# Kernel optimization log

Hardware: AMD Instinct MI355X
Metric: run time of the kernel (lower is better)

Reference implementation:

```python
import jax, jax.numpy as jnp
import numpy as np

B, T, E, QKV, H = 2, 2048, 1024, 1024, 16
DH = QKV // H
R_LAYER = 2

def rmsnorm(x):
    eps = jnp.finfo(x.dtype).eps
    return x * jax.lax.rsqrt(jnp.mean(x * x, axis=-1, keepdims=True) + eps)

def w_norm(w, n):
    # scale whole matrix so its (unbiased) std matches n**-0.5
    std = jnp.std(w, ddof=1)
    return w * (n ** -0.5 / (std + 1e-8))

def rotary(x, cos, sin):
    d = x.shape[-1] // 2
    x1, x2 = x[..., :d], x[..., d:]
    return jnp.concatenate([x1 * cos + x2 * sin, -x1 * sin + x2 * cos], axis=-1)

def w_split(w):
    w_qkv = w[:3 * QKV]                               # (3*QKV, E)
    w_sw = w[3 * QKV:5 * QKV].reshape(2 * E, QKV)     # (2*E, QKV)
    w_out = w[5 * QKV:]                               # (E, E)
    return w_qkv, w_sw, w_out

def aft(x, w_qkv):
    qkv = rmsnorm(x) @ w_qkv.T                        # (B,T,3*QKV)
    q, k, v = jnp.split(qkv, 3, axis=-1)
    q, k = rmsnorm(q), rmsnorm(k)
    wexp = jnp.exp(k)
    kv_c = jnp.cumsum(wexp * v, axis=1)
    w_c = jnp.cumsum(wexp, axis=1)
    y = jax.nn.sigmoid(q) * kv_c / (w_c + 1e-6)
    return x, y

def tea(x, cos, sin, w_qkv):
    qkv = (rmsnorm(x) @ w_qkv.T).reshape(B, T, H, 3 * DH)
    q, k, v = jnp.split(qkv, 3, axis=-1)              # each (B,T,H,DH)
    q, k = rotary(q, cos, sin), rotary(k, cos, sin)
    q, k = rmsnorm(q), rmsnorm(k)
    q = q.transpose(0, 2, 1, 3)                       # (B,H,T,DH)
    k = k.transpose(0, 2, 1, 3)
    v = v.transpose(0, 2, 1, 3)
    scores = jnp.einsum('bhqd,bhkd->bhqk', q, k) * DH ** -0.5
    mask = jnp.tril(jnp.ones((T, T), dtype=bool))
    scores = jnp.where(mask, scores, -jnp.inf)
    att = jax.nn.softmax(scores, axis=-1)
    y = jnp.einsum('bhqk,bhkd->bhqd', att, v)
    return x, y.transpose(0, 2, 1, 3).reshape(B, T, QKV)

def swiglu(x, y, w_sw, w_out, ret_oa=True):
    uv = y @ w_sw.T                                   # (B,T,2*E)
    u, v = jnp.split(uv, 2, axis=-1)
    out = x + (u * jax.nn.silu(v)) @ w_out.T
    if not ret_oa:
        return out
    o = rmsnorm(u.reshape(B * T, -1))
    a = v.reshape(B * T, -1)
    oa = jax.nn.softmax((o.T @ a) * E ** -0.5, axis=-1)  # (E,E)
    return out, oa

def setup_inputs():
    key = jax.random.key(0)
    k1, k2 = jax.random.split(key)
    x = jax.random.normal(k1, (B, T, E), dtype=jnp.float32)
    s = 3 ** 0.5 * E ** -0.5
    w = jax.random.uniform(k2, (5 * QKV + E, E), dtype=jnp.float32, minval=-s, maxval=s)
    half = DH // 2
    inv_freq = 1.0 / (10000.0 ** (jnp.arange(half, dtype=jnp.float32) / half))
    freqs = jnp.outer(jnp.arange(T, dtype=jnp.float32), inv_freq)  # (T, half)
    cos = jnp.cos(freqs)[:, None, :]                  # (T,1,half) broadcasts over (B,T,H,half)
    sin = jnp.sin(freqs)[:, None, :]
    return {"x": x, "w": w, "cos": cos, "sin": sin}

def reference(x, w, cos, sin):
    for i in range(R_LAYER):
        w_qkv, w_sw, w_out = w_split(w)
        w_qkv = w_norm(w_qkv, E)
        w_sw = w_norm(w_sw, QKV)
        w_out = w_norm(w_out, E)
        if (i + 1) % 4 == 0:
            x, y = tea(x, cos, sin, w_qkv)
        else:
            x, y = aft(x, w_qkv)
        x, oa = swiglu(x, y, w_sw, w_out, ret_oa=True)
        # RetentionMechanism.forward: hypernetwork weight mixing
        wT = w_norm(w @ oa, 5 * QKV + E)
        w = wT * jax.nn.silu(w) + w
    w_qkv, w_sw, w_out = w_split(w)                   # note: no w_norm on final split (matches source)
    x, y = tea(x, cos, sin, w_qkv)
    return swiglu(x, y, w_sw, w_out, ret_oa=False)
```

## Files before the change

### kernel.cpp

```cpp
#include <hip/hip_runtime.h>
#include <hip/hip_bf16.h>
#include <math.h>

#define TPB 256

constexpr int Bc = 2, Tc = 2048, Ec = 1024, QKVc = 1024, Hc = 16, DHc = 64;
constexpr long BT = (long)Bc * Tc;
constexpr int WR = 5 * QKVc + Ec;
constexpr float F32_EPS = 1.1920928955078125e-07f;
constexpr int NCH = 64, CHL = Tc / NCH;

typedef __attribute__((ext_vector_type(8))) short short8;
typedef __attribute__((ext_vector_type(4))) float f32x4;

__device__ __forceinline__ unsigned short f2bu(float f) {
    union { __hip_bfloat16 h; unsigned short u; } c; c.h = __float2bfloat16(f); return c.u;
}
__device__ __forceinline__ float bu2f(unsigned short u) {
    union { __hip_bfloat16 h; unsigned short u; } c; c.u = u; return __bfloat162float(c.h);
}
__device__ __forceinline__ float ldval(const float* p) { return *p; }
__device__ __forceinline__ float ldval(const unsigned short* p) { return bu2f(*p); }

__device__ __forceinline__ void gload_lds16(const void* g, void* l) {
    __builtin_amdgcn_global_load_lds((const __attribute__((address_space(1))) void*)g,
                                     (__attribute__((address_space(3))) void*)l, 16, 0, 0);
}

template<int CTRL>
__device__ __forceinline__ float dppf(float x) {
    union { float f; int i; } a, b;
    a.f = x;
    b.i = __builtin_amdgcn_update_dpp(0, a.i, CTRL, 0xF, 0xF, true);
    return b.f;
}
__device__ __forceinline__ float max16(float v) {
    v = fmaxf(v, dppf<0xB1>(v));
    v = fmaxf(v, dppf<0x4E>(v));
    v = fmaxf(v, dppf<0x124>(v));
    v = fmaxf(v, dppf<0x128>(v));
    return v;
}
__device__ __forceinline__ float sum16(float v) {
    v += dppf<0xB1>(v);
    v += dppf<0x4E>(v);
    v += dppf<0x124>(v);
    v += dppf<0x128>(v);
    return v;
}

__global__ void k_std_partial3(const float* __restrict__ w, float* __restrict__ out) {
    __shared__ float ls[TPB], lss[TPB];
    int seg = blockIdx.y;
    long base = (seg == 0) ? 0L : (seg == 1 ? 3072L * 1024 : 5120L * 1024);
    long n    = (seg == 0) ? 3072L * 1024 : (seg == 1 ? 2048L * 1024 : 1024L * 1024);
    const float* p = w + base;
    float s = 0.f, ss = 0.f;
    for (long i = (long)blockIdx.x * TPB + threadIdx.x; i < n; i += 256L * TPB) {
        float v = p[i]; s += v; ss += v * v;
    }
    ls[threadIdx.x] = s; lss[threadIdx.x] = ss; __syncthreads();
    for (int o = 128; o > 0; o >>= 1) {
        if (threadIdx.x < o) { ls[threadIdx.x] += ls[threadIdx.x + o]; lss[threadIdx.x] += lss[threadIdx.x + o]; }
        __syncthreads();
    }
    if (threadIdx.x == 0) { out[seg * 512 + blockIdx.x] = ls[0]; out[seg * 512 + 256 + blockIdx.x] = lss[0]; }
}

__global__ void k_std_final3(const float* __restrict__ part, float* __restrict__ scales) {
    __shared__ float ls[TPB], lss[TPB];
    for (int seg = 0; seg < 3; ++seg) {
        ls[threadIdx.x] = part[seg * 512 + threadIdx.x];
        lss[threadIdx.x] = part[seg * 512 + 256 + threadIdx.x];
        __syncthreads();
        for (int o = 128; o > 0; o >>= 1) {
            if (threadIdx.x < o) { ls[threadIdx.x] += ls[threadIdx.x + o]; lss[threadIdx.x] += lss[threadIdx.x + o]; }
            __syncthreads();
        }
        if (threadIdx.x == 0) {
            float n = (seg == 0) ? 3145728.0f : (seg == 1 ? 2097152.0f : 1048576.0f);
            float var = (lss[0] - ls[0] * ls[0] / n) / (n - 1.0f);
            scales[seg] = 0.03125f / (sqrtf(fmaxf(var, 0.0f)) + 1e-8f);
        }
        __syncthreads();
    }
}

__global__ void k_std_partial(const float* __restrict__ p, long n, float* __restrict__ out) {
    __shared__ float ls[TPB], lss[TPB];
    float s = 0.f, ss = 0.f;
    for (long i = (long)blockIdx.x * TPB + threadIdx.x; i < n; i += (long)gridDim.x * TPB) {
        float v = p[i]; s += v; ss += v * v;
    }
    ls[threadIdx.x] = s; lss[threadIdx.x] = ss; __syncthreads();
    for (int o = 128; o > 0; o >>= 1) {
        if (threadIdx.x < o) { ls[threadIdx.x] += ls[threadIdx.x + o]; lss[threadIdx.x] += lss[threadIdx.x + o]; }
        __syncthreads();
    }
    if (threadIdx.x == 0) { out[blockIdx.x] = ls[0]; out[gridDim.x + blockIdx.x] = lss[0]; }
}

__global__ void k_std_final(const float* __restrict__ part, float n, float rs, float* __restrict__ scale) {
    __shared__ float ls[TPB], lss[TPB];
    ls[threadIdx.x] = part[threadIdx.x];
    lss[threadIdx.x] = part[TPB + threadIdx.x];
    __syncthreads();
    for (int o = 128; o > 0; o >>= 1) {
        if (threadIdx.x < o) { ls[threadIdx.x] += ls[threadIdx.x + o]; lss[threadIdx.x] += lss[threadIdx.x + o]; }
        __syncthreads();
    }
    if (threadIdx.x == 0) {
        float var = (lss[0] - ls[0] * ls[0] / n) / (n - 1.0f);
        scale[0] = rs / (sqrtf(fmaxf(var, 0.0f)) + 1e-8f);
    }
}

__global__ void k_rms_qk(unsigned short* __restrict__ qkv) {
    __shared__ float red[TPB];
    int bid = blockIdx.x;
    long row = bid >> 1; int half = bid & 1;
    unsigned short* p = qkv + row * 3072 + half * 1024;
    ushort4 v = *(const ushort4*)(p + threadIdx.x * 4);
    float f0 = bu2f(v.x), f1 = bu2f(v.y), f2 = bu2f(v.z), f3 = bu2f(v.w);
    red[threadIdx.x] = f0 * f0 + f1 * f1 + f2 * f2 + f3 * f3;
    __syncthreads();
    for (int o = 128; o > 0; o >>= 1) {
        if (threadIdx.x < o) red[threadIdx.x] += red[threadIdx.x + o];
        __syncthreads();
    }
    float sc = rsqrtf(red[0] / 1024.0f + F32_EPS);
    ushort4 o4; o4.x = f2bu(f0 * sc); o4.y = f2bu(f1 * sc); o4.z = f2bu(f2 * sc); o4.w = f2bu(f3 * sc);
    *(ushort4*)(p + threadIdx.x * 4) = o4;
}

__global__ void k_rms1024b(const float* __restrict__ in, unsigned short* __restrict__ out, long ldin, long ldout) {
    __shared__ float red[TPB];
    long row = blockIdx.x;
    float4 v = *(const float4*)(in + row * ldin + threadIdx.x * 4);
    float ss = v.x * v.x + v.y * v.y + v.z * v.z + v.w * v.w;
    red[threadIdx.x] = ss; __syncthreads();
    for (int o = 128; o > 0; o >>= 1) {
        if (threadIdx.x < o) red[threadIdx.x] += red[threadIdx.x + o];
        __syncthreads();
    }
    float sc = rsqrtf(red[0] / 1024.0f + F32_EPS);
    ushort4 o4; o4.x = f2bu(v.x * sc); o4.y = f2bu(v.y * sc); o4.z = f2bu(v.z * sc); o4.w = f2bu(v.w * sc);
    *(ushort4*)(out + row * ldout + threadIdx.x * 4) = o4;
}

__global__ void k_cast_bf16(const float* __restrict__ in, unsigned short* __restrict__ out, long n4) {
    long i = (long)blockIdx.x * TPB + threadIdx.x;
    if (i >= n4) return;
    float4 v = *(const float4*)(in + i * 4);
    ushort4 o; o.x = f2bu(v.x); o.y = f2bu(v.y); o.z = f2bu(v.z); o.w = f2bu(v.w);
    *(ushort4*)(out + i * 4) = o;
}

template<typename TI>
__global__ void k_tcast(const TI* __restrict__ in, long ldi, long sIn,
                        unsigned short* __restrict__ out, long ldo, long sOut,
                        const float* __restrict__ rowscale) {
    __shared__ float tile[64][65];
    const TI* ip = in + (long)blockIdx.z * sIn;
    unsigned short* op = out + (long)blockIdx.z * sOut;
    int r0 = blockIdx.y * 64, c0 = blockIdx.x * 64;
    int tid = threadIdx.x;
    int rr = tid >> 4, cc = (tid & 15) * 4;
    #pragma unroll
    for (int u = 0; u < 4; ++u) {
        int r = rr + u * 16;
        float sc = rowscale ? rowscale[r0 + r] : 1.0f;
        #pragma unroll
        for (int j = 0; j < 4; ++j)
            tile[r][cc + j] = ldval(ip + (long)(r0 + r) * ldi + c0 + cc + j) * sc;
    }
    __syncthreads();
    #pragma unroll
    for (int u = 0; u < 4; ++u) {
        int c = rr + u * 16;
        ushort4 o;
        o.x = f2bu(tile[cc + 0][c]); o.y = f2bu(tile[cc + 1][c]);
        o.z = f2bu(tile[cc + 2][c]); o.w = f2bu(tile[cc + 3][c]);
        *(ushort4*)(op + (long)(c0 + c) * ldo + r0 + cc) = o;
    }
}

__global__ void k_tcast2(const unsigned short* __restrict__ uv, const float* __restrict__ uscale,
                         unsigned short* __restrict__ t1, unsigned short* __restrict__ t2) {
    __shared__ float tile[64][65];
    int z = blockIdx.z;
    const unsigned short* ip = uv + (z ? 1024 : 0);
    unsigned short* op = z ? t2 : t1;
    int r0 = blockIdx.y * 64, c0 = blockIdx.x * 64;
    int tid = threadIdx.x;
    int rr = tid >> 4, cc = (tid & 15) * 4;
    #pragma unroll
    for (int u = 0; u < 4; ++u) {
        int r = rr + u * 16;
        float sc = z ? 1.0f : uscale[r0 + r];
        ushort4 v = *(const ushort4*)(ip + (long)(r0 + r) * 2048 + c0 + cc);
        tile[r][cc + 0] = bu2f(v.x) * sc; tile[r][cc + 1] = bu2f(v.y) * sc;
        tile[r][cc + 2] = bu2f(v.z) * sc; tile[r][cc + 3] = bu2f(v.w) * sc;
    }
    __syncthreads();
    #pragma unroll
    for (int u = 0; u < 4; ++u) {
        int c = rr + u * 16;
        ushort4 o;
        o.x = f2bu(tile[cc + 0][c]); o.y = f2bu(tile[cc + 1][c]);
        o.z = f2bu(tile[cc + 2][c]); o.w = f2bu(tile[cc + 3][c]);
        *(ushort4*)(op + (long)(c0 + c) * 4096 + r0 + cc) = o;
    }
}

template<int WRITE_BF16>
__global__ __launch_bounds__(256)
void k_bgemm(int K,
             const unsigned short* __restrict__ A, int lda, long sA,
             const unsigned short* __restrict__ B, int ldb, long sB,
             void* __restrict__ C, int ldc, long sCi, long sSplit, int nsplit,
             const float* __restrict__ scale_ptr, float fscale,
             const float* __restrict__ addp, int ldadd) {
    __shared__ unsigned short Asl[128 * 64];
    __shared__ unsigned short Bsl[128 * 64];
    int bz = blockIdx.z;
    int batch = bz, sp = 0;
    if (nsplit > 1) { batch = bz / nsplit; sp = bz - batch * nsplit; }
    int m0 = blockIdx.y * 128, n0 = blockIdx.x * 128;
    const unsigned short* Ap = A + (long)batch * sA + (long)sp * K;
    const unsigned short* Bp = B + (long)batch * sB + (long)sp * K;
    int tid = threadIdx.x, lane = tid & 63, wave = tid >> 6;
    int wr = wave >> 1, wc = wave & 1;
    f32x4 acc[4][4] = {};
    for (int k0 = 0; k0 < K; k0 += 64) {
        #pragma unroll
        for (int cc = 0; cc < 4; ++cc) {
            int bu = (wave * 4 + cc) * 64;
            int uidx = bu + lane;
            int r = uidx >> 3, slot = uidx & 7;
            int gu = slot ^ (r & 7);
            gload_lds16(Ap + (long)(m0 + r) * lda + k0 + gu * 8, Asl + bu * 8);
        }
        #pragma unroll
        for (int cc = 0; cc < 4; ++cc) {
            int bu = (wave * 4 + cc) * 64;
            int uidx = bu + lane;
            int r = uidx >> 3, slot = uidx & 7;
            int gu = slot ^ (r & 7);
            gload_lds16(Bp + (long)(n0 + r) * ldb + k0 + gu * 8, Bsl + bu * 8);
        }
        __syncthreads();
        #pragma unroll
        for (int ksub = 0; ksub < 2; ++ksub) {
            short8 av[4], bv[4];
            #pragma unroll
            for (int m = 0; m < 4; ++m) {
                int r = wr * 64 + m * 16 + (lane & 15);
                int slot = (ksub * 4 + (lane >> 4)) ^ (r & 7);
                av[m] = *(const short8*)(Asl + r * 64 + slot * 8);
            }
            #pragma unroll
            for (int n = 0; n < 4; ++n) {
                int r = wc * 64 + n * 16 + (lane & 15);
                int slot = (ksub * 4 + (lane >> 4)) ^ (r & 7);
                bv[n] = *(const short8*)(Bsl + r * 64 + slot * 8);
            }
            #pragma unroll
            for (int m = 0; m < 4; ++m)
                #pragma unroll
                for (int n = 0; n < 4; ++n)
                    acc[m][n] = __builtin_amdgcn_mfma_f32_16x16x32_bf16(av[m], bv[n], acc[m][n], 0, 0, 0);
        }
        __syncthreads();
    }
    float s = fscale * (scale_ptr ? scale_ptr[0] : 1.0f);
    long cbase = (long)batch * sCi + (long)sp * sSplit;
    int row0 = m0 + wr * 64, col0 = n0 + wc * 64 + (lane & 15);
    int rbase = (lane >> 4) * 4;
    #pragma unroll
    for (int m = 0; m < 4; ++m)
        #pragma unroll
        for (int i = 0; i < 4; ++i) {
            long row = row0 + m * 16 + rbase + i;
            #pragma unroll
            for (int n = 0; n < 4; ++n) {
                long col = col0 + n * 16;
                float v = acc[m][n][i] * s;
                if (addp) v += addp[row * (long)ldadd + col];
                long idx = cbase + row * ldc + col;
                if (WRITE_BF16) ((unsigned short*)C)[idx] = f2bu(v);
                else ((float*)C)[idx] = v;
            }
        }
}

__global__ __launch_bounds__(256)
void k_flash_split(const unsigned short* __restrict__ hq, const unsigned short* __restrict__ hk,
                   const unsigned short* __restrict__ hvT,
                   unsigned short* __restrict__ opart, float* __restrict__ mpart, float* __restrict__ lpart) {
    __shared__ unsigned short P_lds[4][32 * 72];
    int lane = threadIdx.x & 63, wave = threadIdx.x >> 6;
    unsigned short* P = P_lds[wave];
    int g = lane >> 4, c = lane & 15;
    unsigned bid = blockIdx.x;
    unsigned bswz = (bid & 7) * 160 + (bid >> 3);
    unsigned gi = bswz * 4 + wave;
    unsigned bh = gi / 160, itr = gi % 160;
    int item = 159 - (int)itr;
    int strip, chunk;
    if (item < 16)      { strip = item;                 chunk = 0; }
    else if (item < 48) { strip = 16 + (item - 16) / 2; chunk = (item - 16) & 1; }
    else if (item < 96) { strip = 32 + (item - 48) / 3; chunk = (item - 48) % 3; }
    else                { strip = 48 + (item - 96) / 4; chunk = (item - 96) & 3; }
    int q0 = strip * 32;
    int nt = (q0 + 32 + 63) >> 6;
    int ti0 = chunk * 8;
    int ti1 = ti0 + 8 < nt ? ti0 + 8 : nt;
    const unsigned short* qb = hq + (long)bh * Tc * 64;
    const unsigned short* kb = hk + (long)bh * Tc * 64;
    const unsigned short* vtb = hvT + (long)bh * 64 * Tc;

    short8 qf[2][2];
    #pragma unroll
    for (int mf = 0; mf < 2; ++mf)
        #pragma unroll
        for (int ks = 0; ks < 2; ++ks)
            qf[mf][ks] = *(const short8*)(qb + (long)(q0 + mf * 16 + c) * 64 + ks * 32 + g * 8);

    f32x4 o_acc[2][4] = {};
    float m_run[2][4], lpp[2][4];
    #pragma unroll
    for (int mf = 0; mf < 2; ++mf)
        #pragma unroll
        for (int i = 0; i < 4; ++i) { m_run[mf][i] = -3.0e38f; lpp[mf][i] = 0.f; }

    short8 kcur[2][4];
    #pragma unroll
    for (int ks = 0; ks < 2; ++ks)
        #pragma unroll
        for (int nf = 0; nf < 4; ++nf)
            kcur[ks][nf] = *(const short8*)(kb + (long)(ti0 * 64 + nf * 16 + c) * 64 + ks * 32 + g * 8);

    for (int ti = ti0; ti < ti1; ++ti) {
        int kt = ti * 64;
        short8 vf[2][4];
        #pragma unroll
        for (int ks = 0; ks < 2; ++ks)
            #pragma unroll
            for (int df = 0; df < 4; ++df)
                vf[ks][df] = *(const short8*)(vtb + (long)(df * 16 + c) * Tc + kt + ks * 32 + g * 8);
        f32x4 s_acc[2][4] = {};
        #pragma unroll
        for (int ks = 0; ks < 2; ++ks)
            #pragma unroll
            for (int mf = 0; mf < 2; ++mf)
                #pragma unroll
                for (int nf = 0; nf < 4; ++nf)
                    s_acc[mf][nf] = __builtin_amdgcn_mfma_f32_16x16x32_bf16(qf[mf][ks], kcur[ks][nf], s_acc[mf][nf], 0, 0, 0);
        short8 knxt[2][4];
        bool more = (ti + 1 < ti1);
        if (more) {
            int kt2 = kt + 64;
            #pragma unroll
            for (int ks = 0; ks < 2; ++ks)
                #pragma unroll
                for (int nf = 0; nf < 4; ++nf)
                    knxt[ks][nf] = *(const short8*)(kb + (long)(kt2 + nf * 16 + c) * 64 + ks * 32 + g * 8);
        }
        if (ti == nt - 1) {
            #pragma unroll
            for (int mf = 0; mf < 2; ++mf)
                #pragma unroll
                for (int nf = 0; nf < 4; ++nf)
                    #pragma unroll
                    for (int i = 0; i < 4; ++i)
                        if ((kt + nf * 16 + c) > (q0 + mf * 16 + g * 4 + i)) s_acc[mf][nf][i] = -1.0e30f;
        }
        float pm[2][4];
        #pragma unroll
        for (int mf = 0; mf < 2; ++mf)
            #pragma unroll
            for (int i = 0; i < 4; ++i)
                pm[mf][i] = max16(fmaxf(fmaxf(s_acc[mf][0][i], s_acc[mf][1][i]),
                                        fmaxf(s_acc[mf][2][i], s_acc[mf][3][i])));
        float mg = 0.f;
        #pragma unroll
        for (int mf = 0; mf < 2; ++mf)
            #pragma unroll
            for (int i = 0; i < 4; ++i) {
                pm[mf][i] *= 0.125f;
                mg = fmaxf(mg, pm[mf][i] - m_run[mf][i]);
            }
        if (__any(mg > 8.0f)) {
            #pragma unroll
            for (int mf = 0; mf < 2; ++mf)
                #pragma unroll
                for (int i = 0; i < 4; ++i) {
                    float mn = fmaxf(m_run[mf][i], pm[mf][i]);
                    float corr = __expf(m_run[mf][i] - mn);
                    m_run[mf][i] = mn;
                    lpp[mf][i] *= corr;
                    #pragma unroll
                    for (int df = 0; df < 4; ++df) o_acc[mf][df][i] *= corr;
                }
        }
        #pragma unroll
        for (int mf = 0; mf < 2; ++mf)
            #pragma unroll
            for (int nf = 0; nf < 4; ++nf)
                #pragma unroll
                for (int i = 0; i < 4; ++i) {
                    float p = __expf(fmaf(s_acc[mf][nf][i], 0.125f, -m_run[mf][i]));
                    P[(mf * 16 + g * 4 + i) * 72 + nf * 16 + c] = f2bu(p);
                    lpp[mf][i] += p;
                }
        #pragma unroll
        for (int ks = 0; ks < 2; ++ks) {
            short8 pa[2];
            #pragma unroll
            for (int mf = 0; mf < 2; ++mf)
                pa[mf] = *(const short8*)(P + (mf * 16 + c) * 72 + ks * 32 + g * 8);
            #pragma unroll
            for (int mf = 0; mf < 2; ++mf)
                #pragma unroll
                for (int df = 0; df < 4; ++df)
                    o_acc[mf][df] = __builtin_amdgcn_mfma_f32_16x16x32_bf16(pa[mf], vf[ks][df], o_acc[mf][df], 0, 0, 0);
        }
        if (more) {
            #pragma unroll
            for (int ks = 0; ks < 2; ++ks)
                #pragma unroll
                for (int nf = 0; nf < 4; ++nf)
                    kcur[ks][nf] = knxt[ks][nf];
        }
    }
    #pragma unroll
    for (int mf = 0; mf < 2; ++mf)
        #pragma unroll
        for (int i = 0; i < 4; ++i)
            lpp[mf][i] = sum16(lpp[mf][i]);
    long pbase = (long)(bh * 160 + item);
    #pragma unroll
    for (int mf = 0; mf < 2; ++mf)
        #pragma unroll
        for (int i = 0; i < 4; ++i) {
            int row_l = mf * 16 + g * 4 + i;
            #pragma unroll
            for (int df = 0; df < 4; ++df)
                opart[pbase * 2048 + row_l * 64 + df * 16 + c] = f2bu(o_acc[mf][df][i]);
            if (c == 0) {
                mpart[pbase * 32 + row_l] = m_run[mf][i];
                lpart[pbase * 32 + row_l] = lpp[mf][i];
            }
        }
}

__global__ __launch_bounds__(256)
void k_flash_merge(const unsigned short* __restrict__ opart, const float* __restrict__ mpart,
                   const float* __restrict__ lpart, unsigned short* __restrict__ yout) {
    int bs = blockIdx.x;
    int bh = bs >> 6, strip = bs & 63;
    int b = bh >> 4, h = bh & 15;
    int np, base;
    if (strip < 16)      { np = 1; base = strip; }
    else if (strip < 32) { np = 2; base = 16 + (strip - 16) * 2; }
    else if (strip < 48) { np = 3; base = 48 + (strip - 32) * 3; }
    else                 { np = 4; base = 96 + (strip - 48) * 4; }
    long p0 = (long)(bh * 160 + base);
    int tid = threadIdx.x;
    int r = tid >> 3, c0 = (tid & 7) * 8;
    float M = -3.0e38f;
    for (int p = 0; p < np; ++p) M = fmaxf(M, mpart[(p0 + p) * 32 + r]);
    float L = 0.f;
    float acc[8] = {};
    for (int p = 0; p < np; ++p) {
        float sc = __expf(mpart[(p0 + p) * 32 + r] - M);
        L += lpart[(p0 + p) * 32 + r] * sc;
        const unsigned short* op = opart + (p0 + p) * 2048 + r * 64 + c0;
        ushort4 a = *(const ushort4*)op;
        ushort4 bq = *(const ushort4*)(op + 4);
        acc[0] += bu2f(a.x) * sc; acc[1] += bu2f(a.y) * sc;
        acc[2] += bu2f(a.z) * sc; acc[3] += bu2f(a.w) * sc;
        acc[4] += bu2f(bq.x) * sc; acc[5] += bu2f(bq.y) * sc;
        acc[6] += bu2f(bq.z) * sc; acc[7] += bu2f(bq.w) * sc;
    }
    float inv = 1.0f / L;
    long row = (long)b * Tc + strip * 32 + r;
    unsigned short* yp = yout + row * 1024 + h * 64 + c0;
    ushort4 o1, o2;
    o1.x = f2bu(acc[0] * inv); o1.y = f2bu(acc[1] * inv); o1.z = f2bu(acc[2] * inv); o1.w = f2bu(acc[3] * inv);
    o2.x = f2bu(acc[4] * inv); o2.y = f2bu(acc[5] * inv); o2.z = f2bu(acc[6] * inv); o2.w = f2bu(acc[7] * inv);
    *(ushort4*)yp = o1;
    *(ushort4*)(yp + 4) = o2;
}

__global__ void k_aft_p1(const unsigned short* __restrict__ qkv, float* __restrict__ cw, float* __restrict__ cs) {
    int id = blockIdx.x * TPB + threadIdx.x;
    int bc = id & 2047, ch = id >> 11;
    int b = bc >> 10, c = bc & 1023;
    const unsigned short* base = qkv + ((long)(b * Tc + ch * CHL)) * 3072 + c;
    float sw = 0.f, sv = 0.f;
    for (int i = 0; i < CHL; ++i) {
        float k = bu2f(base[1024]), v = bu2f(base[2048]);
        float e = __expf(k);
        sw += e; sv += e * v;
        base += 3072;
    }
    cw[ch * 2048 + bc] = sw; cs[ch * 2048 + bc] = sv;
}

__global__ void k_aft_p3(const unsigned short* __restrict__ qkv, const float* __restrict__ cw,
                         const float* __restrict__ cs, unsigned short* __restrict__ y) {
    int id = blockIdx.x * TPB + threadIdx.x;
    int bc = id & 2047, ch = id >> 11;
    int b = bc >> 10, c = bc & 1023;
    float aw = 0.f, av = 0.f;
    for (int cc = 0; cc < ch; ++cc) { aw += cw[cc * 2048 + bc]; av += cs[cc * 2048 + bc]; }
    long t0 = (long)b * Tc + ch * CHL;
    const unsigned short* base = qkv + t0 * 3072 + c;
    unsigned short* yp = y + t0 * 1024 + c;
    for (int i = 0; i < CHL; ++i) {
        float q = bu2f(base[0]), k = bu2f(base[1024]), v = bu2f(base[2048]);
        float e = __expf(k);
        av += e * v; aw += e;
        float sig = 1.0f / (1.0f + __expf(-q));
        yp[0] = f2bu(sig * av / (aw + 1e-6f));
        base += 3072; yp += 1024;
    }
}

__global__ void k_silu_rms(const unsigned short* __restrict__ uv, unsigned short* __restrict__ g,
                           float* __restrict__ rs) {
    __shared__ float red[TPB];
    long row = blockIdx.x;
    const unsigned short* up = uv + row * 2048;
    ushort4 u4 = *(const ushort4*)(up + threadIdx.x * 4);
    ushort4 v4 = *(const ushort4*)(up + 1024 + threadIdx.x * 4);
    float u0 = bu2f(u4.x), u1 = bu2f(u4.y), u2 = bu2f(u4.z), u3 = bu2f(u4.w);
    float v0 = bu2f(v4.x), v1 = bu2f(v4.y), v2 = bu2f(v4.z), v3 = bu2f(v4.w);
    ushort4 o;
    o.x = f2bu(u0 * v0 / (1.f + __expf(-v0)));
    o.y = f2bu(u1 * v1 / (1.f + __expf(-v1)));
    o.z = f2bu(u2 * v2 / (1.f + __expf(-v2)));
    o.w = f2bu(u3 * v3 / (1.f + __expf(-v3)));
    *(ushort4*)(g + row * 1024 + threadIdx.x * 4) = o;
    red[threadIdx.x] = u0 * u0 + u1 * u1 + u2 * u2 + u3 * u3;
    __syncthreads();
    for (int off = 128; off > 0; off >>= 1) {
        if (threadIdx.x < off) red[threadIdx.x] += red[threadIdx.x + off];
        __syncthreads();
    }
    if (threadIdx.x == 0) rs[row] = rsqrtf(red[0] / 1024.0f + F32_EPS);
}

__global__ void k_silu_gate(const unsigned short* __restrict__ uv, unsigned short* __restrict__ g, long n4) {
    long i = (long)blockIdx.x * TPB + threadIdx.x;
    if (i >= n4) return;
    long r = i >> 8, c4 = i & 255;
    ushort4 u4 = *(const ushort4*)(uv + r * 2048 + c4 * 4);
    ushort4 v4 = *(const ushort4*)(uv + r * 2048 + 1024 + c4 * 4);
    float u0 = bu2f(u4.x), u1 = bu2f(u4.y), u2 = bu2f(u4.z), u3 = bu2f(u4.w);
    float v0 = bu2f(v4.x), v1 = bu2f(v4.y), v2 = bu2f(v4.z), v3 = bu2f(v4.w);
    ushort4 o;
    o.x = f2bu(u0 * v0 / (1.f + __expf(-v0)));
    o.y = f2bu(u1 * v1 / (1.f + __expf(-v1)));
    o.z = f2bu(u2 * v2 / (1.f + __expf(-v2)));
    o.w = f2bu(u3 * v3 / (1.f + __expf(-v3)));
    *(ushort4*)(g + r * 1024 + c4 * 4) = o;
}

__global__ void k_wupdate(float* __restrict__ wout, const float* __restrict__ win,
                          const float* __restrict__ p, const float* __restrict__ scale,
                          unsigned short* __restrict__ wb, long n4) {
    long i = (long)blockIdx.x * TPB + threadIdx.x;
    if (i >= n4) return;
    float s = scale[0];
    float4 wv = *(const float4*)(win + i * 4);
    float4 pv = *(const float4*)(p + i * 4);
    float4 o;
    o.x = pv.x * s * (wv.x / (1.f + __expf(-wv.x))) + wv.x;
    o.y = pv.y * s * (wv.y / (1.f + __expf(-wv.y))) + wv.y;
    o.z = pv.z * s * (wv.z / (1.f + __expf(-wv.z))) + wv.z;
    o.w = pv.w * s * (wv.w / (1.f + __expf(-wv.w))) + wv.w;
    *(float4*)(wout + i * 4) = o;
    ushort4 ob; ob.x = f2bu(o.x); ob.y = f2bu(o.y); ob.z = f2bu(o.z); ob.w = f2bu(o.w);
    *(ushort4*)(wb + i * 4) = ob;
}

__global__ void k_softmax4(const float* __restrict__ parts, float* __restrict__ outb, float fscale) {
    __shared__ float red[TPB];
    __shared__ float rowbuf[1024];
    long row = blockIdx.x;
    const float* p0 = parts + row * 1024;
    for (int c = threadIdx.x; c < 1024; c += TPB) {
        float v = p0[c] + p0[c + 1048576] + p0[c + 2097152] + p0[c + 3145728];
        rowbuf[c] = v * fscale;
    }
    __syncthreads();
    float m = -3.0e38f;
    for (int c = threadIdx.x; c < 1024; c += TPB) m = fmaxf(m, rowbuf[c]);
    red[threadIdx.x] = m; __syncthreads();
    for (int o = 128; o > 0; o >>= 1) {
        if (threadIdx.x < o) red[threadIdx.x] = fmaxf(red[threadIdx.x], red[threadIdx.x + o]);
        __syncthreads();
    }
    m = red[0]; __syncthreads();
    float sum = 0.f;
    for (int c = threadIdx.x; c < 1024; c += TPB) sum += __expf(rowbuf[c] - m);
    red[threadIdx.x] = sum; __syncthreads();
    for (int o = 128; o > 0; o >>= 1) {
        if (threadIdx.x < o) red[threadIdx.x] += red[threadIdx.x + o];
        __syncthreads();
    }
    float inv = 1.0f / red[0];
    for (int c = threadIdx.x; c < 1024; c += TPB)
        outb[row * 1024 + c] = __expf(rowbuf[c] - m) * inv;
}

__global__ void k_rot_split(const unsigned short* __restrict__ qkvp, const float* __restrict__ cosp,
                            const float* __restrict__ sinp, unsigned short* __restrict__ hq,
                            unsigned short* __restrict__ hk, unsigned short* __restrict__ hv) {
    __shared__ float row[3072];
    __shared__ float cs[32], sn[32];
    int bt = blockIdx.x;
    int b = bt >> 11, t = bt & 2047;
    const unsigned short* src = qkvp + (long)bt * 3072;
    #pragma unroll
    for (int u = 0; u < 3; ++u) {
        int idx = threadIdx.x + u * 256;
        ushort4 v = *(const ushort4*)(src + idx * 4);
        row[idx * 4 + 0] = bu2f(v.x); row[idx * 4 + 1] = bu2f(v.y);
        row[idx * 4 + 2] = bu2f(v.z); row[idx * 4 + 3] = bu2f(v.w);
    }
    if (threadIdx.x < 32) { cs[threadIdx.x] = cosp[t * 32 + threadIdx.x]; sn[threadIdx.x] = sinp[t * 32 + threadIdx.x]; }
    __syncthreads();
    int h = threadIdx.x >> 4, li = threadIdx.x & 15;
    int base = h * 192;
    long obase = ((long)(b * Hc + h) * Tc + t) * 64 + li * 4;
    {
        float r[4]; float ss = 0.f;
        #pragma unroll
        for (int j = 0; j < 4; ++j) {
            int d = li * 4 + j;
            float val = (d < 32) ? (row[base + d] * cs[d] + row[base + d + 32] * sn[d])
                                 : (-row[base + d - 32] * sn[d - 32] + row[base + d] * cs[d - 32]);
            r[j] = val; ss += val * val;
        }
        ss = sum16(ss);
        float sc = rsqrtf(ss / 64.0f + F32_EPS);
        ushort4 o; o.x = f2bu(r[0] * sc); o.y = f2bu(r[1] * sc); o.z = f2bu(r[2] * sc); o.w = f2bu(r[3] * sc);
        *(ushort4*)(hq + obase) = o;
    }
    {
        int kb = base + 64;
        float r[4]; float ss = 0.f;
        #pragma unroll
        for (int j = 0; j < 4; ++j) {
            int d = li * 4 + j;
            float val = (d < 32) ? (row[kb + d] * cs[d] + row[kb + d + 32] * sn[d])
                                 : (-row[kb + d - 32] * sn[d - 32] + row[kb + d] * cs[d - 32]);
            r[j] = val; ss += val * val;
        }
        ss = sum16(ss);
        float sc = rsqrtf(ss / 64.0f + F32_EPS);
        ushort4 o; o.x = f2bu(r[0] * sc); o.y = f2bu(r[1] * sc); o.z = f2bu(r[2] * sc); o.w = f2bu(r[3] * sc);
        *(ushort4*)(hk + obase) = o;
    }
    {
        ushort4 o;
        o.x = f2bu(row[base + 128 + li * 4 + 0]); o.y = f2bu(row[base + 128 + li * 4 + 1]);
        o.z = f2bu(row[base + 128 + li * 4 + 2]); o.w = f2bu(row[base + 128 + li * 4 + 3]);
        *(ushort4*)(hv + obase) = o;
    }
}

extern "C" void kernel_launch(void* const* d_in, const int* in_sizes, int n_in,
                              void* d_out, int out_size, void* d_ws, size_t ws_size,
                              hipStream_t stream) {
    const float* x_in = (const float*)d_in[0];
    const float* w_in = (const float*)d_in[1];
    const float* cos_in = (const float*)d_in[2];
    const float* sin_in = (const float*)d_in[3];
    float* out = (float*)d_out;
    float* ws = (float*)d_ws;

    long off = 0;
    float* w_cur = ws + off;  off += (long)WR * Ec;
    float* w_tmp = ws + off;  off += (long)WR * Ec;
    float* xbuf  = ws + off;  off += BT * Ec;
    float* R     = ws + off;  off += BT * 3L * QKVc;
    float* oab   = ws + off;  off += (long)Ec * Ec;
    float* red   = ws + off;  off += 2048;
    float* scales= ws + off;  off += 16;
    float* uscale= ws + off;  off += 4096;
    float* chw   = ws + off;  off += 2048L * NCH;
    float* chs   = ws + off;  off += 2048L * NCH;
    unsigned short* qkvb  = (unsigned short*)R;
    unsigned short* uvb   = qkvb + 12582912L;
    unsigned short* opartb= qkvb;
    float* mpart = oab;
    float* lpart = oab + 5120L * 32;

    unsigned short* bp = (unsigned short*)(ws + off);
    long bo = 0;
    unsigned short* wb  = bp + bo; bo += (long)WR * Ec;
    unsigned short* xbn = bp + bo; bo += BT * Ec;
    unsigned short* ybn = bp + bo; bo += BT * Ec;
    unsigned short* gbn = bp + bo; bo += BT * Ec;
    unsigned short* t1  = bp + bo; bo += BT * Ec;
    unsigned short* t2  = bp + bo; bo += BT * Ec;
    unsigned short* t3  = bp + bo; bo += BT * Ec;
    unsigned short* t4  = bp + bo; bo += BT * Ec;

    const float rsWR = 1.0f / sqrtf(6144.0f);
    const long wsw = 3072L * 1024, wout = 5120L * 1024;

    k_cast_bf16<<<(int)(((long)WR * Ec / 4) / TPB), TPB, 0, stream>>>(w_in, wb, (long)WR * Ec / 4);

    for (int layer = 0; layer < 2; ++layer) {
        const float* wsrc = layer == 0 ? w_in : w_cur;
        const float* xsrc = layer == 0 ? x_in : xbuf;
        k_std_partial3<<<dim3(256, 3), TPB, 0, stream>>>(wsrc, red);
        k_std_final3<<<1, TPB, 0, stream>>>(red, scales);
        k_rms1024b<<<BT, TPB, 0, stream>>>(xsrc, xbn, 1024, 1024);
        k_bgemm<1><<<dim3(24, 32, 1), TPB, 0, stream>>>(
            1024, xbn, 1024, 0, wb, 1024, 0, qkvb, 3072, 0, 0, 1, scales + 0, 1.0f, nullptr, 0);
        k_rms_qk<<<8192, TPB, 0, stream>>>(qkvb);
        k_aft_p1<<<(2048 * NCH) / TPB, TPB, 0, stream>>>(qkvb, chw, chs);
        k_aft_p3<<<(2048 * NCH) / TPB, TPB, 0, stream>>>(qkvb, chw, chs, ybn);
        k_bgemm<1><<<dim3(16, 32, 1), TPB, 0, stream>>>(
            1024, ybn, 1024, 0, wb + wsw, 1024, 0, uvb, 2048, 0, 0, 1, scales + 1, 1.0f, nullptr, 0);
        k_silu_rms<<<BT, TPB, 0, stream>>>(uvb, gbn, uscale);
        k_tcast2<<<dim3(16, 64, 2), TPB, 0, stream>>>(uvb, uscale, t1, t2);
        k_bgemm<0><<<dim3(8, 8, 4), TPB, 0, stream>>>(
            1024, t1, 4096, 0, t2, 4096, 0, w_tmp, 1024, 0, 1048576L, 4, nullptr, 1.0f, nullptr, 0);
        k_softmax4<<<1024, TPB, 0, stream>>>(w_tmp, oab, 0.03125f);
        k_tcast<float><<<dim3(16, 16, 1), TPB, 0, stream>>>(oab, 1024, 0, t3, 1024, 0, nullptr);
        k_bgemm<0><<<dim3(8, 32, 1), TPB, 0, stream>>>(
            1024, gbn, 1024, 0, wb + wout, 1024, 0, xbuf, 1024, 0, 0, 1, scales + 2, 1.0f, xsrc, 1024);
        k_bgemm<0><<<dim3(8, 48, 1), TPB, 0, stream>>>(
            1024, wb, 1024, 0, t3, 1024, 0, w_tmp, 1024, 0, 0, 1, nullptr, 1.0f, nullptr, 0);
        k_std_partial<<<256, TPB, 0, stream>>>(w_tmp, (long)WR * 1024, red);
        k_std_final<<<1, TPB, 0, stream>>>(red, (float)((long)WR * 1024), rsWR, scales + 3);
        k_wupdate<<<(int)(((long)WR * 1024 / 4) / TPB), TPB, 0, stream>>>(
            w_cur, wsrc, w_tmp, scales + 3, wb, (long)WR * 1024 / 4);
    }

    k_rms1024b<<<BT, TPB, 0, stream>>>(xbuf, xbn, 1024, 1024);
    k_bgemm<1><<<dim3(24, 32, 1), TPB, 0, stream>>>(
        1024, xbn, 1024, 0, wb, 1024, 0, qkvb, 3072, 0, 0, 1, nullptr, 1.0f, nullptr, 0);
    k_rot_split<<<BT, TPB, 0, stream>>>(qkvb, cos_in, sin_in, t1, t2, t3);
    k_tcast<unsigned short><<<dim3(1, 32, 32), TPB, 0, stream>>>(
        t3, 64, (long)Tc * 64, t4, 2048, (long)Tc * 64, nullptr);
    k_flash_split<<<dim3(1280), TPB, 0, stream>>>(t1, t2, t4, opartb, mpart, lpart);
    k_flash_merge<<<dim3(2048), TPB, 0, stream>>>(opartb, mpart, lpart, ybn);
    k_bgemm<1><<<dim3(16, 32, 1), TPB, 0, stream>>>(
        1024, ybn, 1024, 0, wb + wsw, 1024, 0, uvb, 2048, 0, 0, 1, nullptr, 1.0f, nullptr, 0);
    k_silu_gate<<<(int)((BT * 1024 / 4) / TPB), TPB, 0, stream>>>(uvb, gbn, BT * 1024 / 4);
    k_bgemm<0><<<dim3(8, 32, 1), TPB, 0, stream>>>(
        1024, gbn, 1024, 0, wb + wout, 1024, 0, out, 1024, 0, 0, 1, nullptr, 1.0f, xbuf, 1024);
}
```

Baseline: 825.9 us.

## Split-K the out and weight-mix GEMMs, add AFT chunk prefix pass, simplify flash K loads

The output-projection and w@oa GEMMs become split-K over two halves. Each half writes bf16 partials, and a new merge kernel sums them and adds the residual, which doubles grid parallelism for these small-grid GEMMs. The AFT chunk prefix is computed once in a new p2 kernel, so p3 no longer re-sums all earlier chunks per thread. The flash kernel drops K double-buffering in favour of per-ks loads and adds an occupancy launch bound. The cost is extra partial-buffer traffic and an extra bf16 rounding of GEMM partials, including on the weight-update path.

```diff
diff --git a/kernel.cpp b/kernel.cpp
--- a/kernel.cpp
+++ b/kernel.cpp
@@ -154,6 +154,22 @@
     float4 v = *(const float4*)(in + i * 4);
     ushort4 o; o.x = f2bu(v.x); o.y = f2bu(v.y); o.z = f2bu(v.z); o.w = f2bu(v.w);
     *(ushort4*)(out + i * 4) = o;
+}
+
+__global__ void k_merge2(const unsigned short* __restrict__ p0, const unsigned short* __restrict__ p1,
+                         const float* __restrict__ resid, float* __restrict__ outp, long n4) {
+    long i = (long)blockIdx.x * TPB + threadIdx.x;
+    if (i >= n4) return;
+    ushort4 a = *(const ushort4*)(p0 + i * 4);
+    ushort4 b = *(const ushort4*)(p1 + i * 4);
+    float4 o;
+    o.x = bu2f(a.x) + bu2f(b.x); o.y = bu2f(a.y) + bu2f(b.y);
+    o.z = bu2f(a.z) + bu2f(b.z); o.w = bu2f(a.w) + bu2f(b.w);
+    if (resid) {
+        float4 r = *(const float4*)(resid + i * 4);
+        o.x += r.x; o.y += r.y; o.z += r.z; o.w += r.w;
+    }
+    *(float4*)(outp + i * 4) = o;
 }
 
 template<typename TI>
@@ -294,7 +310,7 @@
         }
 }
 
-__global__ __launch_bounds__(256)
+__global__ __launch_bounds__(256, 4)
 void k_flash_split(const unsigned short* __restrict__ hq, const unsigned short* __restrict__ hk,
                    const unsigned short* __restrict__ hvT,
                    unsigned short* __restrict__ opart, float* __restrict__ mpart, float* __restrict__ lpart) {
@@ -334,13 +350,6 @@
         #pragma unroll
         for (int i = 0; i < 4; ++i) { m_run[mf][i] = -3.0e38f; lpp[mf][i] = 0.f; }
 
-    short8 kcur[2][4];
-    #pragma unroll
-    for (int ks = 0; ks < 2; ++ks)
-        #pragma unroll
-        for (int nf = 0; nf < 4; ++nf)
-            kcur[ks][nf] = *(const short8*)(kb + (long)(ti0 * 64 + nf * 16 + c) * 64 + ks * 32 + g * 8);
-
     for (int ti = ti0; ti < ti1; ++ti) {
         int kt = ti * 64;
         short8 vf[2][4];
@@ -351,21 +360,16 @@
                 vf[ks][df] = *(const short8*)(vtb + (long)(df * 16 + c) * Tc + kt + ks * 32 + g * 8);
         f32x4 s_acc[2][4] = {};
         #pragma unroll
-        for (int ks = 0; ks < 2; ++ks)
+        for (int ks = 0; ks < 2; ++ks) {
+            short8 kf[4];
+            #pragma unroll
+            for (int nf = 0; nf < 4; ++nf)
+                kf[nf] = *(const short8*)(kb + (long)(kt + nf * 16 + c) * 64 + ks * 32 + g * 8);
             #pragma unroll
             for (int mf = 0; mf < 2; ++mf)
                 #pragma unroll
                 for (int nf = 0; nf < 4; ++nf)
-                    s_acc[mf][nf] = __builtin_amdgcn_mfma_f32_16x16x32_bf16(qf[mf][ks], kcur[ks][nf], s_acc[mf][nf], 0, 0, 0);
-        short8 knxt[2][4];
-        bool more = (ti + 1 < ti1);
-        if (more) {
-            int kt2 = kt + 64;
-            #pragma unroll
-            for (int ks = 0; ks < 2; ++ks)
-                #pragma unroll
-                for (int nf = 0; nf < 4; ++nf)
-                    knxt[ks][nf] = *(const short8*)(kb + (long)(kt2 + nf * 16 + c) * 64 + ks * 32 + g * 8);
+                    s_acc[mf][nf] = __builtin_amdgcn_mfma_f32_16x16x32_bf16(qf[mf][ks], kf[nf], s_acc[mf][nf], 0, 0, 0);
         }
         if (ti == nt - 1) {
             #pragma unroll
@@ -425,13 +429,6 @@
                 #pragma unroll
                 for (int df = 0; df < 4; ++df)
                     o_acc[mf][df] = __builtin_amdgcn_mfma_f32_16x16x32_bf16(pa[mf], vf[ks][df], o_acc[mf][df], 0, 0, 0);
-        }
-        if (more) {
-            #pragma unroll
-            for (int ks = 0; ks < 2; ++ks)
-                #pragma unroll
-                for (int nf = 0; nf < 4; ++nf)
-                    kcur[ks][nf] = knxt[ks][nf];
         }
     }
     #pragma unroll
@@ -509,13 +506,22 @@
     cw[ch * 2048 + bc] = sw; cs[ch * 2048 + bc] = sv;
 }
 
+__global__ void k_aft_p2(float* __restrict__ cw, float* __restrict__ cs) {
+    int bc = blockIdx.x * TPB + threadIdx.x;
+    float rw = 0.f, rv = 0.f;
+    for (int ch = 0; ch < NCH; ++ch) {
+        long idx = (long)ch * 2048 + bc;
+        float tw = cw[idx], tv = cs[idx];
+        cw[idx] = rw; cs[idx] = rv; rw += tw; rv += tv;
+    }
+}
+
 __global__ void k_aft_p3(const unsigned short* __restrict__ qkv, const float* __restrict__ cw,
                          const float* __restrict__ cs, unsigned short* __restrict__ y) {
     int id = blockIdx.x * TPB + threadIdx.x;
     int bc = id & 2047, ch = id >> 11;
     int b = bc >> 10, c = bc & 1023;
-    float aw = 0.f, av = 0.f;
-    for (int cc = 0; cc < ch; ++cc) { aw += cw[cc * 2048 + bc]; av += cs[cc * 2048 + bc]; }
+    float aw = cw[ch * 2048 + bc], av = cs[ch * 2048 + bc];
     long t0 = (long)b * Tc + ch * CHL;
     const unsigned short* base = qkv + t0 * 3072 + c;
     unsigned short* yp = y + t0 * 1024 + c;
@@ -698,6 +704,8 @@
     unsigned short* qkvb  = (unsigned short*)R;
     unsigned short* uvb   = qkvb + 12582912L;
     unsigned short* opartb= qkvb;
+    unsigned short* wsplit = qkvb;
+    unsigned short* osplit = uvb;
     float* mpart = oab;
     float* lpart = oab + 5120L * 32;
 
@@ -727,6 +735,7 @@
             1024, xbn, 1024, 0, wb, 1024, 0, qkvb, 3072, 0, 0, 1, scales + 0, 1.0f, nullptr, 0);
         k_rms_qk<<<8192, TPB, 0, stream>>>(qkvb);
         k_aft_p1<<<(2048 * NCH) / TPB, TPB, 0, stream>>>(qkvb, chw, chs);
+        k_aft_p2<<<2048 / TPB, TPB, 0, stream>>>(chw, chs);
         k_aft_p3<<<(2048 * NCH) / TPB, TPB, 0, stream>>>(qkvb, chw, chs, ybn);
         k_bgemm<1><<<dim3(16, 32, 1), TPB, 0, stream>>>(
             1024, ybn, 1024, 0, wb + wsw, 1024, 0, uvb, 2048, 0, 0, 1, scales + 1, 1.0f, nullptr, 0);
@@ -736,10 +745,14 @@
             1024, t1, 4096, 0, t2, 4096, 0, w_tmp, 1024, 0, 1048576L, 4, nullptr, 1.0f, nullptr, 0);
         k_softmax4<<<1024, TPB, 0, stream>>>(w_tmp, oab, 0.03125f);
         k_tcast<float><<<dim3(16, 16, 1), TPB, 0, stream>>>(oab, 1024, 0, t3, 1024, 0, nullptr);
-        k_bgemm<0><<<dim3(8, 32, 1), TPB, 0, stream>>>(
-            1024, gbn, 1024, 0, wb + wout, 1024, 0, xbuf, 1024, 0, 0, 1, scales + 2, 1.0f, xsrc, 1024);
-        k_bgemm<0><<<dim3(8, 48, 1), TPB, 0, stream>>>(
-            1024, wb, 1024, 0, t3, 1024, 0, w_tmp, 1024, 0, 0, 1, nullptr, 1.0f, nullptr, 0);
+        k_bgemm<1><<<dim3(8, 32, 2), TPB, 0, stream>>>(
+            512, gbn, 1024, 0, wb + wout, 1024, 0, osplit, 1024, 0, 4194304L, 2, scales + 2, 1.0f, nullptr, 0);
+        k_merge2<<<(int)((BT * 1024 / 4) / TPB), TPB, 0, stream>>>(
+            osplit, osplit + 4194304L, xsrc, xbuf, BT * 1024 / 4);
+        k_bgemm<1><<<dim3(8, 48, 2), TPB, 0, stream>>>(
+            512, wb, 1024, 0, t3, 1024, 0, wsplit, 1024, 0, 6291456L, 2, nullptr, 1.0f, nullptr, 0);
+        k_merge2<<<(int)(((long)WR * 1024 / 4) / TPB), TPB, 0, stream>>>(
+            wsplit, wsplit + 6291456L, nullptr, w_tmp, (long)WR * 1024 / 4);
         k_std_partial<<<256, TPB, 0, stream>>>(w_tmp, (long)WR * 1024, red);
         k_std_final<<<1, TPB, 0, stream>>>(red, (float)((long)WR * 1024), rsWR, scales + 3);
         k_wupdate<<<(int)(((long)WR * 1024 / 4) / TPB), TPB, 0, stream>>>(
@@ -757,6 +770,8 @@
     k_bgemm<1><<<dim3(16, 32, 1), TPB, 0, stream>>>(
         1024, ybn, 1024, 0, wb + wsw, 1024, 0, uvb, 2048, 0, 0, 1, nullptr, 1.0f, nullptr, 0);
     k_silu_gate<<<(int)((BT * 1024 / 4) / TPB), TPB, 0, stream>>>(uvb, gbn, BT * 1024 / 4);
-    k_bgemm<0><<<dim3(8, 32, 1), TPB, 0, stream>>>(
-        1024, gbn, 1024, 0, wb + wout, 1024, 0, out, 1024, 0, 0, 1, nullptr, 1.0f, xbuf, 1024);
-}
+    k_bgemm<1><<<dim3(8, 32, 2), TPB, 0, stream>>>(
+        512, gbn, 1024, 0, wb + wout, 1024, 0, qkvb, 1024, 0, 4194304L, 2, nullptr, 1.0f, nullptr, 0);
+    k_merge2<<<(int)((BT * 1024 / 4) / TPB), TPB, 0, stream>>>(
+        qkvb, qkvb + 4194304L, xbuf, out, BT * 1024 / 4);
+}
```

After: 865.0 us. +4.7%, slower.
